# Kernel optimization log

Hardware: AMD Instinct MI355X
Metric: run time of the kernel (lower is better)

## Reference

```python
import jax, jax.numpy as jnp
import numpy as np

NUM_CLASSES = 80
NUM_PRIORS = 3
STRIDES = (8, 16, 32)
ANCHORS = (((10, 13), (16, 30), (33, 23)),
           ((30, 61), (62, 45), (59, 119)),
           ((116, 90), (156, 198), (373, 326)))
PRE_TOP_K = 1000
KEEP_TOP_K = 100
IOU_THR = 0.65
SCORE_THR = 0.25
IMG = 640
CLS_OFFSET = 4096.0  # class-offset trick for batched (class-aware) NMS


def _make_priors():
    priors, strides = [], []
    for lvl, s in enumerate(STRIDES):
        fs = IMG // s
        ys, xs = np.meshgrid(np.arange(fs), np.arange(fs), indexing='ij')
        cx = (xs * s).astype(np.float32)[..., None]
        cy = (ys * s).astype(np.float32)[..., None]
        anc = np.asarray(ANCHORS[lvl], np.float32)  # [3,2]
        cx = np.broadcast_to(cx, (fs, fs, NUM_PRIORS))
        cy = np.broadcast_to(cy, (fs, fs, NUM_PRIORS))
        w = np.broadcast_to(anc[None, None, :, 0], (fs, fs, NUM_PRIORS))
        h = np.broadcast_to(anc[None, None, :, 1], (fs, fs, NUM_PRIORS))
        box = np.stack([cx - w / 2, cy - h / 2, cx + w / 2, cy + h / 2], -1).reshape(-1, 4)
        priors.append(box)
        strides.append(np.full((box.shape[0],), s, np.float32))
    return jnp.asarray(np.concatenate(priors)), jnp.asarray(np.concatenate(strides))


def setup_inputs() -> dict:
    key = jax.random.key(0)
    ks = jax.random.split(key, 9)
    shapes = {
        'cls0': (32, 240, 80, 80), 'cls1': (32, 240, 40, 40), 'cls2': (32, 240, 20, 20),
        'bbox0': (32, 12, 80, 80), 'bbox1': (32, 12, 40, 40), 'bbox2': (32, 12, 20, 20),
        'obj0': (32, 3, 80, 80), 'obj1': (32, 3, 40, 40), 'obj2': (32, 3, 20, 20),
    }
    inp = {n: jax.random.normal(k, s, dtype=jnp.float32) for (n, s), k in zip(shapes.items(), ks)}
    priors, strides = _make_priors()
    inp['priors'] = priors
    inp['strides'] = strides
    return inp


def _flatten(x, last):  # [B,C,H,W] -> [B, H*W*priors, last]
    B = x.shape[0]
    return jnp.transpose(x, (0, 2, 3, 1)).reshape(B, -1, last)


def _decode_yolov5(priors, preds, strides):
    # priors [N,4] (x1,y1,x2,y2), preds [B,N,4], strides [N]
    p = jax.nn.sigmoid(preds)
    cx = (priors[:, 0] + priors[:, 2]) * 0.5
    cy = (priors[:, 1] + priors[:, 3]) * 0.5
    w = priors[:, 2] - priors[:, 0]
    h = priors[:, 3] - priors[:, 1]
    xc = (p[..., 0] - 0.5) * 2.0 * strides + cx
    yc = (p[..., 1] - 0.5) * 2.0 * strides + cy
    wp = (p[..., 2] * 2.0) ** 2 * w
    hp = (p[..., 3] * 2.0) ** 2 * h
    return jnp.stack([xc - wp * 0.5, yc - hp * 0.5, xc + wp * 0.5, yc + hp * 0.5], -1)


def _pairwise_iou(b):  # b [K,4]
    area = (b[:, 2] - b[:, 0]) * (b[:, 3] - b[:, 1])
    lt = jnp.maximum(b[:, None, :2], b[None, :, :2])
    rb = jnp.minimum(b[:, None, 2:], b[None, :, 2:])
    wh = jnp.clip(rb - lt, 0.0)
    inter = wh[..., 0] * wh[..., 1]
    return inter / (area[:, None] + area[None, :] - inter + 1e-7)


def _nms_single(boxes, scores):
    # boxes [N,4], scores [N,C]
    flat = scores.reshape(-1)
    top_s, top_i = jax.lax.top_k(flat, PRE_TOP_K)  # sorted desc
    anchor = top_i // NUM_CLASSES
    label = top_i % NUM_CLASSES
    b = boxes[anchor]  # [K,4]
    bo = b + label.astype(boxes.dtype)[:, None] * CLS_OFFSET
    iou = _pairwise_iou(bo)
    valid = top_s > SCORE_THR
    idxs = jnp.arange(PRE_TOP_K)

    def body(i, supp):
        keep_i = jnp.logical_not(supp[i])
        return jnp.where(keep_i & (iou[i] > IOU_THR) & (idxs > i), True, supp)

    supp = jax.lax.fori_loop(0, PRE_TOP_K, body, jnp.logical_not(valid))
    keep = jnp.logical_not(supp) & valid
    k_scores = jnp.where(keep, top_s, 0.0)
    det_s, det_i = jax.lax.top_k(k_scores, KEEP_TOP_K)
    det_b = b[det_i]
    det_l = label[det_i]
    num = jnp.minimum(jnp.sum(keep.astype(jnp.int32)), KEEP_TOP_K)
    return num, det_b, det_s, det_l


def reference(cls0, cls1, cls2, bbox0, bbox1, bbox2, obj0, obj1, obj2, priors, strides):
    cls = jnp.concatenate([_flatten(c, NUM_CLASSES) for c in (cls0, cls1, cls2)], axis=1)
    scores = jax.nn.sigmoid(cls)  # [B,N,C]
    bp = jnp.concatenate([_flatten(b, 4) for b in (bbox0, bbox1, bbox2)], axis=1)
    obj = jnp.concatenate([_flatten(o, 1)[..., 0] for o in (obj0, obj1, obj2)], axis=1)
    scores = scores * jax.nn.sigmoid(obj)[..., None]
    bboxes = _decode_yolov5(priors, bp, strides)  # [B,N,4]
    num, det_b, det_s, det_l = jax.vmap(_nms_single)(bboxes, scores)
    return num, det_b, det_s, det_l
```

## Files before the change

### kernel.cpp

```cpp
#include <hip/hip_runtime.h>
#include <stdint.h>

#define NCLS 80
#define CELLS 8400
#define PRE 1000
#define KEEP 100
#define CAP 4096
#define NBINS 16384
#define NIMG 32
#define SUBS 8
#define SUBCAP 2048
#define GBINS 4096
#define COMPCAP 2048
#define T0 0.75f
#define SCREEN 1.0886f

__device__ __forceinline__ float sigm(float x) { return 1.0f / (1.0f + __expf(-x)); }

__device__ __forceinline__ void lvlinfo(int cell, int& li, int& loc, int& HW) {
  if (cell < 6400)      { li = 0; loc = cell;        HW = 6400; }
  else if (cell < 8000) { li = 1; loc = cell - 6400; HW = 1600; }
  else                  { li = 2; loc = cell - 8000; HW = 400;  }
}

__global__ __launch_bounds__(256) void k_pass1(
    const float* __restrict__ cls0, const float* __restrict__ cls1, const float* __restrict__ cls2,
    const float* __restrict__ obj0, const float* __restrict__ obj1, const float* __restrict__ obj2,
    uint32_t* __restrict__ cnt75, uint64_t* __restrict__ cand75) {
  const int b = blockIdx.y;
  const int bx = blockIdx.x;
  const int sb = bx >> 1;
  const int h  = bx & 1;
  const int c0cell = (sb * 256 + threadIdx.x) * 4;
  if (c0cell >= CELLS) return;
  int li, loc, HW; lvlinfo(c0cell, li, loc, HW);
  const float* cls = li == 0 ? cls0 : (li == 1 ? cls1 : cls2);
  const float* obj = li == 0 ? obj0 : (li == 1 ? obj1 : obj2);

  float4 o0 = *(const float4*)(obj + ((size_t)b * 3 + 0) * HW + loc);
  float4 o1 = *(const float4*)(obj + ((size_t)b * 3 + 1) * HW + loc);
  float4 o2 = *(const float4*)(obj + ((size_t)b * 3 + 2) * HW + loc);
  float os[3][4];
  os[0][0] = sigm(o0.x); os[0][1] = sigm(o0.y); os[0][2] = sigm(o0.z); os[0][3] = sigm(o0.w);
  os[1][0] = sigm(o1.x); os[1][1] = sigm(o1.y); os[1][2] = sigm(o1.z); os[1][3] = sigm(o1.w);
  os[2][0] = sigm(o2.x); os[2][1] = sigm(o2.y); os[2][2] = sigm(o2.z); os[2][3] = sigm(o2.w);

  const int sub = bx & (SUBS - 1);
  for (int p = 0; p < 3; ++p) {
    const float* cp = cls + ((size_t)b * 240 + p * 80 + h * 40) * HW + loc;
    for (int gq = 0; gq < 5; ++gq) {
      float4 v[8];
#pragma unroll
      for (int u = 0; u < 8; ++u)
        v[u] = *(const float4*)(cp + (size_t)(gq * 8 + u) * HW);
#pragma unroll
      for (int u = 0; u < 8; ++u) {
        const int c = h * 40 + gq * 8 + u;
        float vv[4] = { v[u].x, v[u].y, v[u].z, v[u].w };
#pragma unroll
        for (int k = 0; k < 4; ++k) {
          if (vv[k] > SCREEN) {
            float s = sigm(vv[k]) * os[p][k];
            if (s > T0) {
              uint32_t slot = atomicAdd(&cnt75[b * SUBS + sub], 1u);
              if (slot < SUBCAP) {
                uint32_t flat = (uint32_t)(((c0cell + k) * 3 + p) * 80 + c);
                cand75[((size_t)(b * SUBS + sub)) * SUBCAP + slot] =
                    ((uint64_t)__float_as_uint(s) << 32) | (uint64_t)(0xFFFFFFFFu - flat);
              }
            }
          }
        }
      }
    }
  }
}

__global__ __launch_bounds__(1024) void k_gather(
    const uint64_t* __restrict__ cand75, const uint32_t* __restrict__ cnt75,
    uint32_t* __restrict__ flags,
    const float* __restrict__ bbox0, const float* __restrict__ bbox1, const float* __restrict__ bbox2,
    const float* __restrict__ priors, const float* __restrict__ strides,
    float* __restrict__ topS, int* __restrict__ topLab, float* __restrict__ topBox,
    uint32_t* __restrict__ nvArr) {
  __shared__ uint32_t hist[GBINS];
  __shared__ uint64_t comp[COMPCAP];
  __shared__ uint32_t seg[64];
  __shared__ uint32_t ncomp_s, cb_s;
  const int b = blockIdx.x;
  const int tid = threadIdx.x;
  uint32_t tot = 0; bool bad = false;
  for (int s = 0; s < SUBS; ++s) {
    uint32_t cc = cnt75[b * SUBS + s];
    tot += cc;
    if (cc > SUBCAP) bad = true;
  }
  if (tot < (uint32_t)PRE) bad = true;
  if (bad) { if (tid == 0) flags[b] = 1u; return; }

  for (int i = tid; i < GBINS; i += 1024) hist[i] = 0;
  if (tid == 0) ncomp_s = 0;
  __syncthreads();
  for (int s = 0; s < SUBS; ++s) {
    uint32_t c = cnt75[b * SUBS + s];
    const uint64_t* src = cand75 + ((size_t)(b * SUBS + s)) * SUBCAP;
    for (int i = tid; i < (int)c; i += 1024) {
      uint32_t hi = (uint32_t)(src[i] >> 32);
      uint32_t bin = (hi - 0x3F400000u) >> 10;
      if (bin > GBINS - 1) bin = GBINS - 1;
      atomicAdd(&hist[bin], 1u);
    }
  }
  __syncthreads();
  if (tid < 64) {
    uint32_t s = 0;
    for (int k = 0; k < 64; ++k) s += hist[tid * 64 + k];
    seg[tid] = s;
  }
  __syncthreads();
  if (tid == 0) {
    uint32_t acc = 0; int segi = 0;
    for (int i = 63; i >= 0; --i) {
      if (acc + seg[i] >= (uint32_t)PRE) { segi = i; break; }
      acc += seg[i];
    }
    uint32_t cb = 0;
    for (int k = 63; k >= 0; --k) {
      acc += hist[segi * 64 + k];
      if (acc >= (uint32_t)PRE) { cb = (uint32_t)(segi * 64 + k); break; }
    }
    cb_s = cb;
  }
  __syncthreads();
  const uint32_t cb = cb_s;
  for (int s = 0; s < SUBS; ++s) {
    uint32_t c = cnt75[b * SUBS + s];
    const uint64_t* src = cand75 + ((size_t)(b * SUBS + s)) * SUBCAP;
    for (int i = tid; i < (int)c; i += 1024) {
      uint64_t key = src[i];
      uint32_t hi = (uint32_t)(key >> 32);
      uint32_t bin = (hi - 0x3F400000u) >> 10;
      if (bin > GBINS - 1) bin = GBINS - 1;
      if (bin >= cb) {
        uint32_t pos = atomicAdd(&ncomp_s, 1u);
        if (pos < COMPCAP) comp[pos] = key;
      }
    }
  }
  __syncthreads();
  const uint32_t ncomp = ncomp_s;
  if (ncomp > COMPCAP) { if (tid == 0) flags[b] = 1u; return; }
  for (int i = tid; i < COMPCAP; i += 1024) if (i >= (int)ncomp) comp[i] = 0ull;
  __syncthreads();
  for (int k = 2; k <= COMPCAP; k <<= 1) {
    for (int j = k >> 1; j > 0; j >>= 1) {
      for (int i = tid; i < COMPCAP; i += 1024) {
        int p = i ^ j;
        if (p > i) {
          uint64_t a = comp[i], c = comp[p];
          bool asc = (i & k) != 0;
          if (asc ? (a > c) : (a < c)) { comp[i] = c; comp[p] = a; }
        }
      }
      __syncthreads();
    }
  }
  if (tid == 0) nvArr[b] = (uint32_t)PRE;
  for (int t = tid; t < PRE; t += 1024) {
    uint64_t key = comp[t];
    float sc = __uint_as_float((uint32_t)(key >> 32));
    uint32_t flat = 0xFFFFFFFFu - (uint32_t)(key & 0xFFFFFFFFull);
    uint32_t n = flat / 80u; int lab = (int)(flat - n * 80u);
    uint32_t g = n / 3u; uint32_t p = n - g * 3u;
    int li, loc, HW; lvlinfo((int)g, li, loc, HW);
    const float* bb = li == 0 ? bbox0 : (li == 1 ? bbox1 : bbox2);
    size_t o = ((size_t)b * 12 + p * 4) * HW + loc;
    float p0 = sigm(bb[o]);
    float p1 = sigm(bb[o + (size_t)HW]);
    float p2 = sigm(bb[o + 2 * (size_t)HW]);
    float p3 = sigm(bb[o + 3 * (size_t)HW]);
    float4 pr = *(const float4*)(priors + (size_t)n * 4);
    float st = strides[n];
    float cx = (pr.x + pr.z) * 0.5f, cy = (pr.y + pr.w) * 0.5f;
    float w = pr.z - pr.x, hh = pr.w - pr.y;
    float xc = (p0 - 0.5f) * 2.0f * st + cx;
    float yc = (p1 - 0.5f) * 2.0f * st + cy;
    float wp = p2 * 2.0f; wp = wp * wp * w;
    float hp = p3 * 2.0f; hp = hp * hp * hh;
    topS[(size_t)b * PRE + t] = sc;
    topLab[(size_t)b * PRE + t] = lab;
    *(float4*)(topBox + ((size_t)b * PRE + t) * 4) =
        make_float4(xc - wp * 0.5f, yc - hp * 0.5f, xc + wp * 0.5f, yc + hp * 0.5f);
  }
}

__global__ __launch_bounds__(256) void k_hist_fb(
    const float* __restrict__ cls0, const float* __restrict__ cls1, const float* __restrict__ cls2,
    const float* __restrict__ obj0, const float* __restrict__ obj1, const float* __restrict__ obj2,
    uint32_t* __restrict__ hist, const uint32_t* __restrict__ flags) {
  const int b = blockIdx.y;
  if (flags[b] == 0u) return;
  __shared__ uint32_t h[NBINS];
  for (int i = threadIdx.x; i < NBINS; i += 256) h[i] = 0;
  __syncthreads();
  const int c0 = (blockIdx.x * 256 + threadIdx.x) * 4;
  if (c0 < CELLS) {
    int li, loc, HW; lvlinfo(c0, li, loc, HW);
    const float* cls = li == 0 ? cls0 : (li == 1 ? cls1 : cls2);
    const float* obj = li == 0 ? obj0 : (li == 1 ? obj1 : obj2);
    float os[3][4];
#pragma unroll
    for (int p = 0; p < 3; ++p) {
      float4 o = *(const float4*)(obj + ((size_t)b * 3 + p) * HW + loc);
      os[p][0] = sigm(o.x); os[p][1] = sigm(o.y); os[p][2] = sigm(o.z); os[p][3] = sigm(o.w);
    }
    for (int p = 0; p < 3; ++p) {
      const float* cp = cls + ((size_t)b * 240 + p * 80) * HW + loc;
      for (int c = 0; c < 80; ++c) {
        float4 v = *(const float4*)(cp + (size_t)c * HW);
        float sv[4] = { sigm(v.x) * os[p][0], sigm(v.y) * os[p][1],
                        sigm(v.z) * os[p][2], sigm(v.w) * os[p][3] };
#pragma unroll
        for (int k = 0; k < 4; ++k) {
          if (sv[k] > 0.25f) {
            uint32_t key = (__float_as_uint(sv[k]) - 0x3E800000u) >> 10;
            if (key > NBINS - 1) key = NBINS - 1;
            atomicAdd(&h[key], 1u);
          }
        }
      }
    }
  }
  __syncthreads();
  for (int i = threadIdx.x; i < NBINS; i += 256) {
    uint32_t v = h[i];
    if (v) atomicAdd(&hist[(size_t)b * NBINS + i], v);
  }
}

__global__ __launch_bounds__(256) void k_cutoff_fb(const uint32_t* __restrict__ hist,
                                                   uint32_t* __restrict__ cutoff,
                                                   const uint32_t* __restrict__ flags) {
  const int b = blockIdx.x;
  if (flags[b] == 0u) return;
  __shared__ uint32_t seg[256];
  const uint32_t* hb = hist + (size_t)b * NBINS;
  uint32_t s = 0;
  for (int k = 0; k < 64; ++k) s += hb[threadIdx.x * 64 + k];
  seg[threadIdx.x] = s;
  __syncthreads();
  if (threadIdx.x == 0) {
    uint32_t acc = 0; int segi = -1;
    for (int i = 255; i >= 0; --i) {
      if (acc + seg[i] >= (uint32_t)PRE) { segi = i; break; }
      acc += seg[i];
    }
    uint32_t cut = 0;
    if (segi >= 0) {
      for (int k = 63; k >= 0; --k) {
        acc += hb[segi * 64 + k];
        if (acc >= (uint32_t)PRE) { cut = (uint32_t)(segi * 64 + k); break; }
      }
    }
    cutoff[b] = cut;
  }
}

__global__ __launch_bounds__(256) void k_collect_fb(
    const float* __restrict__ cls0, const float* __restrict__ cls1, const float* __restrict__ cls2,
    const float* __restrict__ obj0, const float* __restrict__ obj1, const float* __restrict__ obj2,
    const uint32_t* __restrict__ cutoff, uint32_t* __restrict__ candCount,
    uint64_t* __restrict__ cand, const uint32_t* __restrict__ flags) {
  const int b = blockIdx.y;
  if (flags[b] == 0u) return;
  const int c0 = (blockIdx.x * 256 + threadIdx.x) * 4;
  if (c0 >= CELLS) return;
  const uint32_t cut = cutoff[b];
  int li, loc, HW; lvlinfo(c0, li, loc, HW);
  const float* cls = li == 0 ? cls0 : (li == 1 ? cls1 : cls2);
  const float* obj = li == 0 ? obj0 : (li == 1 ? obj1 : obj2);
  float os[3][4];
#pragma unroll
  for (int p = 0; p < 3; ++p) {
    float4 o = *(const float4*)(obj + ((size_t)b * 3 + p) * HW + loc);
    os[p][0] = sigm(o.x); os[p][1] = sigm(o.y); os[p][2] = sigm(o.z); os[p][3] = sigm(o.w);
  }
  for (int p = 0; p < 3; ++p) {
    const float* cp = cls + ((size_t)b * 240 + p * 80) * HW + loc;
    for (int c = 0; c < 80; ++c) {
      float4 v = *(const float4*)(cp + (size_t)c * HW);
      float sv[4] = { sigm(v.x) * os[p][0], sigm(v.y) * os[p][1],
                      sigm(v.z) * os[p][2], sigm(v.w) * os[p][3] };
#pragma unroll
      for (int k = 0; k < 4; ++k) {
        float sk = sv[k];
        if (sk > 0.25f) {
          uint32_t key = (__float_as_uint(sk) - 0x3E800000u) >> 10;
          if (key >= cut) {
            uint32_t pos = atomicAdd(&candCount[b], 1u);
            if (pos < CAP) {
              uint32_t flat = (uint32_t)((((c0 + k) * 3 + p) * 80) + c);
              cand[(size_t)b * CAP + pos] =
                  ((uint64_t)__float_as_uint(sk) << 32) | (uint64_t)(0xFFFFFFFFu - flat);
            }
          }
        }
      }
    }
  }
}

__global__ __launch_bounds__(1024) void k_sort_decode_fb(
    const uint64_t* __restrict__ cand, const uint32_t* __restrict__ candCount,
    const float* __restrict__ bbox0, const float* __restrict__ bbox1, const float* __restrict__ bbox2,
    const float* __restrict__ priors, const float* __restrict__ strides,
    float* __restrict__ topS, int* __restrict__ topLab, float* __restrict__ topBox,
    uint32_t* __restrict__ nvArr, const uint32_t* __restrict__ flags) {
  const int b = blockIdx.x;
  if (flags[b] == 0u) return;
  __shared__ uint64_t s[CAP];
  uint32_t cnt = candCount[b]; if (cnt > (uint32_t)CAP) cnt = CAP;
  for (int i = threadIdx.x; i < CAP; i += 1024)
    s[i] = (i < (int)cnt) ? cand[(size_t)b * CAP + i] : 0ull;
  __syncthreads();
  for (int k = 2; k <= CAP; k <<= 1) {
    for (int j = k >> 1; j > 0; j >>= 1) {
      for (int i = threadIdx.x; i < CAP; i += 1024) {
        int p = i ^ j;
        if (p > i) {
          uint64_t a = s[i], c = s[p];
          bool asc = (i & k) != 0;
          if (asc ? (a > c) : (a < c)) { s[i] = c; s[p] = a; }
        }
      }
      __syncthreads();
    }
  }
  const int NV = (int)(cnt < (uint32_t)PRE ? cnt : (uint32_t)PRE);
  if (threadIdx.x == 0) nvArr[b] = (uint32_t)NV;
  for (int t = threadIdx.x; t < PRE; t += 1024) {
    float sc = 0.0f; int lab = 0; float b0 = 0, b1 = 0, b2v = 0, b3 = 0;
    if (t < NV) {
      uint64_t key = s[t];
      sc = __uint_as_float((uint32_t)(key >> 32));
      uint32_t flat = 0xFFFFFFFFu - (uint32_t)(key & 0xFFFFFFFFull);
      uint32_t n = flat / 80u; lab = (int)(flat - n * 80u);
      uint32_t g = n / 3u; uint32_t p = n - g * 3u;
      int li, loc, HW; lvlinfo((int)g, li, loc, HW);
      const float* bb = li == 0 ? bbox0 : (li == 1 ? bbox1 : bbox2);
      size_t o = ((size_t)b * 12 + p * 4) * HW + loc;
      float p0 = sigm(bb[o]);
      float p1 = sigm(bb[o + (size_t)HW]);
      float p2 = sigm(bb[o + 2 * (size_t)HW]);
      float p3 = sigm(bb[o + 3 * (size_t)HW]);
      float4 pr = *(const float4*)(priors + (size_t)n * 4);
      float st = strides[n];
      float cx = (pr.x + pr.z) * 0.5f, cy = (pr.y + pr.w) * 0.5f;
      float w = pr.z - pr.x, hh = pr.w - pr.y;
      float xc = (p0 - 0.5f) * 2.0f * st + cx;
      float yc = (p1 - 0.5f) * 2.0f * st + cy;
      float wp = p2 * 2.0f; wp = wp * wp * w;
      float hp = p3 * 2.0f; hp = hp * hp * hh;
      b0 = xc - wp * 0.5f; b1 = yc - hp * 0.5f; b2v = xc + wp * 0.5f; b3 = yc + hp * 0.5f;
    }
    topS[(size_t)b * PRE + t] = sc;
    topLab[(size_t)b * PRE + t] = lab;
    *(float4*)(topBox + ((size_t)b * PRE + t) * 4) = make_float4(b0, b1, b2v, b3);
  }
}

__global__ __launch_bounds__(256) void k_iou(
    const float* __restrict__ topBox, const int* __restrict__ topLab,
    const uint32_t* __restrict__ nvArr, uint64_t* __restrict__ mask) {
  __shared__ float4 bx[PRE];
  __shared__ int lb[PRE];
  const int b = blockIdx.y;
  const int NV = (int)nvArr[b];
  for (int i = threadIdx.x; i < PRE; i += 256) {
    bx[i] = *(const float4*)(topBox + ((size_t)b * PRE + i) * 4);
    lb[i] = topLab[(size_t)b * PRE + i];
  }
  __syncthreads();
  for (int task = blockIdx.x * 256 + threadIdx.x; task < PRE * 16; task += gridDim.x * 256) {
    const int i = task >> 4, w = task & 15;
    uint64_t m = 0;
    if (i < NV) {
      const float4 a = bx[i]; const int la = lb[i];
      const float areaA = (a.z - a.x) * (a.w - a.y);
      const int j0 = w << 6;
      const int jend = (j0 + 64 < NV) ? j0 + 64 : NV;
      for (int j = (j0 > i + 1 ? j0 : i + 1); j < jend; ++j) {
        if (lb[j] != la) continue;
        const float4 c = bx[j];
        float xx1 = fmaxf(a.x, c.x), yy1 = fmaxf(a.y, c.y);
        float xx2 = fminf(a.z, c.z), yy2 = fminf(a.w, c.w);
        float iw = fmaxf(xx2 - xx1, 0.0f), ih = fmaxf(yy2 - yy1, 0.0f);
        float inter = iw * ih;
        float areaB = (c.z - c.x) * (c.w - c.y);
        float iou = inter / (areaA + areaB - inter + 1e-7f);
        if (iou > 0.65f) m |= (1ull << (j - j0));
      }
    }
    mask[((size_t)b * PRE + i) * 16 + w] = m;
  }
}

__global__ __launch_bounds__(256) void k_scan_out(
    const uint64_t* __restrict__ mask, const float* __restrict__ topS,
    const int* __restrict__ topLab, const float* __restrict__ topBox,
    const uint32_t* __restrict__ nvArr, float* __restrict__ out) {
  __shared__ uint64_t rows[PRE * 16];
  __shared__ uint64_t keepw[16];
  __shared__ uint32_t pref[17];
  const int b = blockIdx.x;
  const int NV = (int)nvArr[b];
  for (int i = threadIdx.x; i < NV * 16; i += 256) rows[i] = mask[(size_t)b * PRE * 16 + i];
  __syncthreads();
  if (threadIdx.x < 64) {
    const int lane = threadIdx.x;
    uint64_t remv = 0, kw = 0;
    for (int w0 = 0; w0 * 64 < NV; ++w0) {
      uint64_t cur = (uint64_t)__shfl((unsigned long long)remv, w0);
      const int ie = (w0 * 64 + 64 < NV) ? w0 * 64 + 64 : NV;
      for (int i = w0 * 64; i < ie; ++i) {
        const int bi = i & 63;
        if (!((cur >> bi) & 1ull)) {
          uint64_t rl = rows[i * 16 + (lane & 15)];
          cur |= rows[i * 16 + w0];
          if (lane < 16) remv |= rl;
          if (lane == w0) kw |= (1ull << bi);
        }
      }
    }
    if (lane < 16) keepw[lane] = kw;
  }
  __syncthreads();
  if (threadIdx.x == 0) {
    uint32_t a = 0;
    for (int w = 0; w < 16; ++w) { pref[w] = a; a += (uint32_t)__popcll((unsigned long long)keepw[w]); }
    pref[16] = a;
  }
  __syncthreads();
  const uint32_t total = pref[16];
  const uint32_t num = total < (uint32_t)KEEP ? total : (uint32_t)KEEP;
  float* o_num = out;
  float* o_box = out + NIMG;
  float* o_s   = out + NIMG + NIMG * KEEP * 4;
  float* o_l   = o_s + NIMG * KEEP;
  if (threadIdx.x == 0) o_num[b] = (float)num;
  const int zstart = NV < KEEP ? NV : KEEP;
  for (int sidx = zstart + threadIdx.x; sidx < KEEP; sidx += 256) {
    ((float4*)o_box)[b * KEEP + sidx] = make_float4(0, 0, 0, 0);
    o_s[b * KEEP + sidx] = 0.0f;
    o_l[b * KEEP + sidx] = 0.0f;
  }
  for (int j = threadIdx.x; j < NV; j += 256) {
    const int wi = j >> 6, bi = j & 63;
    const uint64_t kword = keepw[wi];
    const int isk = (int)((kword >> bi) & 1ull);
    const uint32_t below = pref[wi] + (uint32_t)__popcll((unsigned long long)(kword & ((1ull << bi) - 1ull)));
    const uint32_t slot = isk ? below : (total + (uint32_t)j - below);
    if (slot < (uint32_t)KEEP) {
      ((float4*)o_box)[b * KEEP + slot] = *(const float4*)(topBox + ((size_t)b * PRE + j) * 4);
      o_s[b * KEEP + slot] = isk ? topS[(size_t)b * PRE + j] : 0.0f;
      o_l[b * KEEP + slot] = (float)topLab[(size_t)b * PRE + j];
    }
  }
}

extern "C" void kernel_launch(void* const* d_in, const int* in_sizes, int n_in,
                              void* d_out, int out_size, void* d_ws, size_t ws_size,
                              hipStream_t stream) {
  (void)in_sizes; (void)n_in; (void)out_size; (void)ws_size;
  const float* cls0 = (const float*)d_in[0];
  const float* cls1 = (const float*)d_in[1];
  const float* cls2 = (const float*)d_in[2];
  const float* bbox0 = (const float*)d_in[3];
  const float* bbox1 = (const float*)d_in[4];
  const float* bbox2 = (const float*)d_in[5];
  const float* obj0 = (const float*)d_in[6];
  const float* obj1 = (const float*)d_in[7];
  const float* obj2 = (const float*)d_in[8];
  const float* priors = (const float*)d_in[9];
  const float* strides = (const float*)d_in[10];
  float* out = (float*)d_out;

  char* ws = (char*)d_ws;
  size_t off = 0;
  auto alloc = [&](size_t bytes) -> void* {
    void* p = ws + off;
    off = (off + bytes + 255) & ~(size_t)255;
    return p;
  };
  uint32_t* small     = (uint32_t*)alloc(4096);
  uint32_t* flags     = small;
  uint32_t* cnt75     = small + 32;
  uint32_t* candCount = small + 288;
  uint32_t* cutoff    = small + 320;
  uint32_t* nvArr     = small + 352;
  uint64_t* cand75    = (uint64_t*)alloc((size_t)NIMG * SUBS * SUBCAP * 8);
  uint32_t* hist      = (uint32_t*)alloc((size_t)NIMG * NBINS * 4);
  uint64_t* cand      = (uint64_t*)alloc((size_t)NIMG * CAP * 8);
  float*    topS      = (float*)alloc((size_t)NIMG * PRE * 4);
  int*      topLab    = (int*)alloc((size_t)NIMG * PRE * 4);
  float*    topBox    = (float*)alloc((size_t)NIMG * PRE * 16);
  uint64_t* maskbuf   = (uint64_t*)alloc((size_t)NIMG * PRE * 16 * 8);

  hipMemsetAsync(small, 0, 4096, stream);
  hipMemsetAsync(hist, 0, (size_t)NIMG * NBINS * 4, stream);

  k_pass1<<<dim3(18, NIMG), 256, 0, stream>>>(cls0, cls1, cls2, obj0, obj1, obj2,
                                              cnt75, cand75);
  k_gather<<<NIMG, 1024, 0, stream>>>(cand75, cnt75, flags, bbox0, bbox1, bbox2,
                                      priors, strides, topS, topLab, topBox, nvArr);
  dim3 gScan(9, NIMG);
  k_hist_fb<<<gScan, 256, 0, stream>>>(cls0, cls1, cls2, obj0, obj1, obj2, hist, flags);
  k_cutoff_fb<<<NIMG, 256, 0, stream>>>(hist, cutoff, flags);
  k_collect_fb<<<gScan, 256, 0, stream>>>(cls0, cls1, cls2, obj0, obj1, obj2,
                                          cutoff, candCount, cand, flags);
  k_sort_decode_fb<<<NIMG, 1024, 0, stream>>>(cand, candCount, bbox0, bbox1, bbox2,
                                              priors, strides, topS, topLab, topBox, nvArr, flags);
  k_iou<<<dim3(63, NIMG), 256, 0, stream>>>(topBox, topLab, nvArr, maskbuf);
  k_scan_out<<<NIMG, 256, 0, stream>>>(maskbuf, topS, topLab, topBox, nvArr, out);
}
```

Baseline: 421.6 us.

## Double-buffer pass1 loads, shrink gather sort, fuse IoU with scan, gate hist zeroing

Pass1 now software-pipelines class-channel loads across two register buffers and skips a group early when its max is below the screen threshold. The gather bitonic sort uses 1024 elements when the candidate count fits. The 2MB histogram memset becomes a kernel that zeroes only when some image needs the fallback path. The IoU-mask and scan kernels are fused into one block per image that keeps the mask in shared memory, which removes a global round-trip but drops from 63x32 blocks to 32 blocks for the IoU work.

```diff
diff --git a/kernel.cpp b/kernel.cpp
--- a/kernel.cpp
+++ b/kernel.cpp
@@ -46,34 +46,41 @@
   os[2][0] = sigm(o2.x); os[2][1] = sigm(o2.y); os[2][2] = sigm(o2.z); os[2][3] = sigm(o2.w);
 
   const int sub = bx & (SUBS - 1);
+
+#define LD(dst, GQ) { _Pragma("unroll") for (int u = 0; u < 8; ++u) \
+    dst[u] = *(const float4*)(cp + (size_t)((GQ) * 8 + u) * HW); }
+#define PR(src, GQ) { \
+    float mx = fmaxf(fmaxf(src[0].x, src[0].y), fmaxf(src[0].z, src[0].w)); \
+    _Pragma("unroll") for (int u = 1; u < 8; ++u) \
+      mx = fmaxf(mx, fmaxf(fmaxf(src[u].x, src[u].y), fmaxf(src[u].z, src[u].w))); \
+    if (mx > SCREEN) { \
+      _Pragma("unroll") for (int u = 0; u < 8; ++u) { \
+        const int c = h * 40 + (GQ) * 8 + u; \
+        float vv[4] = { src[u].x, src[u].y, src[u].z, src[u].w }; \
+        _Pragma("unroll") for (int k = 0; k < 4; ++k) { \
+          if (vv[k] > SCREEN) { \
+            float s = sigm(vv[k]) * os[p][k]; \
+            if (s > T0) { \
+              uint32_t slot = atomicAdd(&cnt75[b * SUBS + sub], 1u); \
+              if (slot < SUBCAP) { \
+                uint32_t flat = (uint32_t)(((c0cell + k) * 3 + p) * 80 + c); \
+                cand75[((size_t)(b * SUBS + sub)) * SUBCAP + slot] = \
+                    ((uint64_t)__float_as_uint(s) << 32) | (uint64_t)(0xFFFFFFFFu - flat); \
+              } } } } } } }
+
+#pragma unroll
   for (int p = 0; p < 3; ++p) {
     const float* cp = cls + ((size_t)b * 240 + p * 80 + h * 40) * HW + loc;
-    for (int gq = 0; gq < 5; ++gq) {
-      float4 v[8];
-#pragma unroll
-      for (int u = 0; u < 8; ++u)
-        v[u] = *(const float4*)(cp + (size_t)(gq * 8 + u) * HW);
-#pragma unroll
-      for (int u = 0; u < 8; ++u) {
-        const int c = h * 40 + gq * 8 + u;
-        float vv[4] = { v[u].x, v[u].y, v[u].z, v[u].w };
-#pragma unroll
-        for (int k = 0; k < 4; ++k) {
-          if (vv[k] > SCREEN) {
-            float s = sigm(vv[k]) * os[p][k];
-            if (s > T0) {
-              uint32_t slot = atomicAdd(&cnt75[b * SUBS + sub], 1u);
-              if (slot < SUBCAP) {
-                uint32_t flat = (uint32_t)(((c0cell + k) * 3 + p) * 80 + c);
-                cand75[((size_t)(b * SUBS + sub)) * SUBCAP + slot] =
-                    ((uint64_t)__float_as_uint(s) << 32) | (uint64_t)(0xFFFFFFFFu - flat);
-              }
-            }
-          }
-        }
-      }
-    }
-  }
+    float4 va[8], vb[8];
+    LD(va, 0)
+    LD(vb, 1) PR(va, 0)
+    LD(va, 2) PR(vb, 1)
+    LD(vb, 3) PR(va, 2)
+    LD(va, 4) PR(vb, 3)
+    PR(va, 4)
+  }
+#undef LD
+#undef PR
 }
 
 __global__ __launch_bounds__(1024) void k_gather(
@@ -150,11 +157,12 @@
   __syncthreads();
   const uint32_t ncomp = ncomp_s;
   if (ncomp > COMPCAP) { if (tid == 0) flags[b] = 1u; return; }
-  for (int i = tid; i < COMPCAP; i += 1024) if (i >= (int)ncomp) comp[i] = 0ull;
-  __syncthreads();
-  for (int k = 2; k <= COMPCAP; k <<= 1) {
+  const int N = (ncomp <= 1024u) ? 1024 : COMPCAP;
+  for (int i = tid; i < N; i += 1024) if (i >= (int)ncomp) comp[i] = 0ull;
+  __syncthreads();
+  for (int k = 2; k <= N; k <<= 1) {
     for (int j = k >> 1; j > 0; j >>= 1) {
-      for (int i = tid; i < COMPCAP; i += 1024) {
+      for (int i = tid; i < N; i += 1024) {
         int p = i ^ j;
         if (p > i) {
           uint64_t a = comp[i], c = comp[p];
@@ -194,6 +202,21 @@
   }
 }
 
+__global__ __launch_bounds__(256) void k_zero_hist(uint32_t* __restrict__ hist,
+                                                   const uint32_t* __restrict__ flags) {
+  __shared__ uint32_t any;
+  if (threadIdx.x == 0) {
+    uint32_t a = 0;
+    for (int i = 0; i < NIMG; ++i) a |= flags[i];
+    any = a;
+  }
+  __syncthreads();
+  if (!any) return;
+  const int total = NIMG * NBINS;
+  for (int i = blockIdx.x * 256 + threadIdx.x; i < total; i += gridDim.x * 256)
+    hist[i] = 0;
+}
+
 __global__ __launch_bounds__(256) void k_hist_fb(
     const float* __restrict__ cls0, const float* __restrict__ cls1, const float* __restrict__ cls2,
     const float* __restrict__ obj0, const float* __restrict__ obj1, const float* __restrict__ obj2,
@@ -369,19 +392,23 @@
   }
 }
 
-__global__ __launch_bounds__(256) void k_iou(
+__global__ __launch_bounds__(256) void k_iou_scan(
     const float* __restrict__ topBox, const int* __restrict__ topLab,
-    const uint32_t* __restrict__ nvArr, uint64_t* __restrict__ mask) {
+    const float* __restrict__ topS, const uint32_t* __restrict__ nvArr,
+    float* __restrict__ out) {
   __shared__ float4 bx[PRE];
   __shared__ int lb[PRE];
-  const int b = blockIdx.y;
+  __shared__ uint64_t rows[PRE * 16];
+  __shared__ uint64_t keepw[16];
+  __shared__ uint32_t pref[17];
+  const int b = blockIdx.x;
   const int NV = (int)nvArr[b];
   for (int i = threadIdx.x; i < PRE; i += 256) {
     bx[i] = *(const float4*)(topBox + ((size_t)b * PRE + i) * 4);
     lb[i] = topLab[(size_t)b * PRE + i];
   }
   __syncthreads();
-  for (int task = blockIdx.x * 256 + threadIdx.x; task < PRE * 16; task += gridDim.x * 256) {
+  for (int task = threadIdx.x; task < PRE * 16; task += 256) {
     const int i = task >> 4, w = task & 15;
     uint64_t m = 0;
     if (i < NV) {
@@ -401,20 +428,8 @@
         if (iou > 0.65f) m |= (1ull << (j - j0));
       }
     }
-    mask[((size_t)b * PRE + i) * 16 + w] = m;
-  }
-}
-
-__global__ __launch_bounds__(256) void k_scan_out(
-    const uint64_t* __restrict__ mask, const float* __restrict__ topS,
-    const int* __restrict__ topLab, const float* __restrict__ topBox,
-    const uint32_t* __restrict__ nvArr, float* __restrict__ out) {
-  __shared__ uint64_t rows[PRE * 16];
-  __shared__ uint64_t keepw[16];
-  __shared__ uint32_t pref[17];
-  const int b = blockIdx.x;
-  const int NV = (int)nvArr[b];
-  for (int i = threadIdx.x; i < NV * 16; i += 256) rows[i] = mask[(size_t)b * PRE * 16 + i];
+    rows[i * 16 + w] = m;
+  }
   __syncthreads();
   if (threadIdx.x < 64) {
     const int lane = threadIdx.x;
@@ -461,9 +476,9 @@
     const uint32_t below = pref[wi] + (uint32_t)__popcll((unsigned long long)(kword & ((1ull << bi) - 1ull)));
     const uint32_t slot = isk ? below : (total + (uint32_t)j - below);
     if (slot < (uint32_t)KEEP) {
-      ((float4*)o_box)[b * KEEP + slot] = *(const float4*)(topBox + ((size_t)b * PRE + j) * 4);
+      ((float4*)o_box)[b * KEEP + slot] = bx[j];
       o_s[b * KEEP + slot] = isk ? topS[(size_t)b * PRE + j] : 0.0f;
-      o_l[b * KEEP + slot] = (float)topLab[(size_t)b * PRE + j];
+      o_l[b * KEEP + slot] = (float)lb[j];
     }
   }
 }
@@ -504,15 +519,14 @@
   float*    topS      = (float*)alloc((size_t)NIMG * PRE * 4);
   int*      topLab    = (int*)alloc((size_t)NIMG * PRE * 4);
   float*    topBox    = (float*)alloc((size_t)NIMG * PRE * 16);
-  uint64_t* maskbuf   = (uint64_t*)alloc((size_t)NIMG * PRE * 16 * 8);
 
   hipMemsetAsync(small, 0, 4096, stream);
-  hipMemsetAsync(hist, 0, (size_t)NIMG * NBINS * 4, stream);
 
   k_pass1<<<dim3(18, NIMG), 256, 0, stream>>>(cls0, cls1, cls2, obj0, obj1, obj2,
                                               cnt75, cand75);
   k_gather<<<NIMG, 1024, 0, stream>>>(cand75, cnt75, flags, bbox0, bbox1, bbox2,
                                       priors, strides, topS, topLab, topBox, nvArr);
+  k_zero_hist<<<256, 256, 0, stream>>>(hist, flags);
   dim3 gScan(9, NIMG);
   k_hist_fb<<<gScan, 256, 0, stream>>>(cls0, cls1, cls2, obj0, obj1, obj2, hist, flags);
   k_cutoff_fb<<<NIMG, 256, 0, stream>>>(hist, cutoff, flags);
@@ -520,6 +534,5 @@
                                           cutoff, candCount, cand, flags);
   k_sort_decode_fb<<<NIMG, 1024, 0, stream>>>(cand, candCount, bbox0, bbox1, bbox2,
                                               priors, strides, topS, topLab, topBox, nvArr, flags);
-  k_iou<<<dim3(63, NIMG), 256, 0, stream>>>(topBox, topLab, nvArr, maskbuf);
-  k_scan_out<<<NIMG, 256, 0, stream>>>(maskbuf, topS, topLab, topBox, nvArr, out);
-}
+  k_iou_scan<<<NIMG, 256, 0, stream>>>(topBox, topLab, topS, nvArr, out);
+}
```

After: 830.1 us. 96.9% more time.

## Split pass1 per prior, shrink bitonic sort, lazy hist zeroing, branchless NMS scan

Applied to the files above, without the earlier changes.

The first pass grid now launches one block per (cell tile, prior, class half), tripling the block count for more parallelism on the bandwidth-bound class scan. The gather bitonic sort runs on 1024 entries when the candidate count fits, halving the sort work. The histogram memset is replaced by a kernel that clears it only when some image took the fallback path. The NMS scan loop becomes branchless with masks. The risks are an extra launch and more obj reloads, and the sub-bucket index now comes from a different block mapping, which could change atomic contention.

```diff
diff --git a/kernel.cpp b/kernel.cpp
--- a/kernel.cpp
+++ b/kernel.cpp
@@ -29,45 +29,40 @@
     uint32_t* __restrict__ cnt75, uint64_t* __restrict__ cand75) {
   const int b = blockIdx.y;
   const int bx = blockIdx.x;
-  const int sb = bx >> 1;
-  const int h  = bx & 1;
+  const int sb = bx / 6;
+  const int r  = bx - sb * 6;
+  const int h  = r & 1;
+  const int p  = r >> 1;
   const int c0cell = (sb * 256 + threadIdx.x) * 4;
   if (c0cell >= CELLS) return;
   int li, loc, HW; lvlinfo(c0cell, li, loc, HW);
   const float* cls = li == 0 ? cls0 : (li == 1 ? cls1 : cls2);
   const float* obj = li == 0 ? obj0 : (li == 1 ? obj1 : obj2);
 
-  float4 o0 = *(const float4*)(obj + ((size_t)b * 3 + 0) * HW + loc);
-  float4 o1 = *(const float4*)(obj + ((size_t)b * 3 + 1) * HW + loc);
-  float4 o2 = *(const float4*)(obj + ((size_t)b * 3 + 2) * HW + loc);
-  float os[3][4];
-  os[0][0] = sigm(o0.x); os[0][1] = sigm(o0.y); os[0][2] = sigm(o0.z); os[0][3] = sigm(o0.w);
-  os[1][0] = sigm(o1.x); os[1][1] = sigm(o1.y); os[1][2] = sigm(o1.z); os[1][3] = sigm(o1.w);
-  os[2][0] = sigm(o2.x); os[2][1] = sigm(o2.y); os[2][2] = sigm(o2.z); os[2][3] = sigm(o2.w);
+  float4 ov = *(const float4*)(obj + ((size_t)b * 3 + p) * HW + loc);
+  float os[4] = { sigm(ov.x), sigm(ov.y), sigm(ov.z), sigm(ov.w) };
 
   const int sub = bx & (SUBS - 1);
-  for (int p = 0; p < 3; ++p) {
-    const float* cp = cls + ((size_t)b * 240 + p * 80 + h * 40) * HW + loc;
-    for (int gq = 0; gq < 5; ++gq) {
-      float4 v[8];
-#pragma unroll
-      for (int u = 0; u < 8; ++u)
-        v[u] = *(const float4*)(cp + (size_t)(gq * 8 + u) * HW);
-#pragma unroll
-      for (int u = 0; u < 8; ++u) {
-        const int c = h * 40 + gq * 8 + u;
-        float vv[4] = { v[u].x, v[u].y, v[u].z, v[u].w };
-#pragma unroll
-        for (int k = 0; k < 4; ++k) {
-          if (vv[k] > SCREEN) {
-            float s = sigm(vv[k]) * os[p][k];
-            if (s > T0) {
-              uint32_t slot = atomicAdd(&cnt75[b * SUBS + sub], 1u);
-              if (slot < SUBCAP) {
-                uint32_t flat = (uint32_t)(((c0cell + k) * 3 + p) * 80 + c);
-                cand75[((size_t)(b * SUBS + sub)) * SUBCAP + slot] =
-                    ((uint64_t)__float_as_uint(s) << 32) | (uint64_t)(0xFFFFFFFFu - flat);
-              }
+  const float* cp = cls + ((size_t)b * 240 + p * 80 + h * 40) * HW + loc;
+  for (int gq = 0; gq < 5; ++gq) {
+    float4 v[8];
+#pragma unroll
+    for (int u = 0; u < 8; ++u)
+      v[u] = *(const float4*)(cp + (size_t)(gq * 8 + u) * HW);
+#pragma unroll
+    for (int u = 0; u < 8; ++u) {
+      const int c = h * 40 + gq * 8 + u;
+      float vv[4] = { v[u].x, v[u].y, v[u].z, v[u].w };
+#pragma unroll
+      for (int k = 0; k < 4; ++k) {
+        if (vv[k] > SCREEN) {
+          float s = sigm(vv[k]) * os[k];
+          if (s > T0) {
+            uint32_t slot = atomicAdd(&cnt75[b * SUBS + sub], 1u);
+            if (slot < SUBCAP) {
+              uint32_t flat = (uint32_t)(((c0cell + k) * 3 + p) * 80 + c);
+              cand75[((size_t)(b * SUBS + sub)) * SUBCAP + slot] =
+                  ((uint64_t)__float_as_uint(s) << 32) | (uint64_t)(0xFFFFFFFFu - flat);
             }
           }
         }
@@ -150,11 +145,12 @@
   __syncthreads();
   const uint32_t ncomp = ncomp_s;
   if (ncomp > COMPCAP) { if (tid == 0) flags[b] = 1u; return; }
-  for (int i = tid; i < COMPCAP; i += 1024) if (i >= (int)ncomp) comp[i] = 0ull;
-  __syncthreads();
-  for (int k = 2; k <= COMPCAP; k <<= 1) {
+  const int N = (ncomp <= 1024u) ? 1024 : COMPCAP;
+  for (int i = tid; i < N; i += 1024) if (i >= (int)ncomp) comp[i] = 0ull;
+  __syncthreads();
+  for (int k = 2; k <= N; k <<= 1) {
     for (int j = k >> 1; j > 0; j >>= 1) {
-      for (int i = tid; i < COMPCAP; i += 1024) {
+      for (int i = tid; i < N; i += 1024) {
         int p = i ^ j;
         if (p > i) {
           uint64_t a = comp[i], c = comp[p];
@@ -194,6 +190,21 @@
   }
 }
 
+__global__ __launch_bounds__(256) void k_zero_hist(uint32_t* __restrict__ hist,
+                                                   const uint32_t* __restrict__ flags) {
+  __shared__ uint32_t any;
+  if (threadIdx.x == 0) {
+    uint32_t a = 0;
+    for (int i = 0; i < NIMG; ++i) a |= flags[i];
+    any = a;
+  }
+  __syncthreads();
+  if (!any) return;
+  const int total = NIMG * NBINS;
+  for (int i = blockIdx.x * 256 + threadIdx.x; i < total; i += gridDim.x * 256)
+    hist[i] = 0;
+}
+
 __global__ __launch_bounds__(256) void k_hist_fb(
     const float* __restrict__ cls0, const float* __restrict__ cls1, const float* __restrict__ cls2,
     const float* __restrict__ obj0, const float* __restrict__ obj1, const float* __restrict__ obj2,
@@ -424,12 +435,12 @@
       const int ie = (w0 * 64 + 64 < NV) ? w0 * 64 + 64 : NV;
       for (int i = w0 * 64; i < ie; ++i) {
         const int bi = i & 63;
-        if (!((cur >> bi) & 1ull)) {
-          uint64_t rl = rows[i * 16 + (lane & 15)];
-          cur |= rows[i * 16 + w0];
-          if (lane < 16) remv |= rl;
-          if (lane == w0) kw |= (1ull << bi);
-        }
+        uint64_t rl = rows[i * 16 + (lane & 15)];
+        uint64_t cw = rows[i * 16 + w0];
+        const uint64_t keepm = ((cur >> bi) & 1ull) ? 0ull : ~0ull;
+        cur |= cw & keepm;
+        remv |= rl & keepm;
+        kw |= (lane == w0) ? ((1ull << bi) & keepm) : 0ull;
       }
     }
     if (lane < 16) keepw[lane] = kw;
@@ -507,12 +518,12 @@
   uint64_t* maskbuf   = (uint64_t*)alloc((size_t)NIMG * PRE * 16 * 8);
 
   hipMemsetAsync(small, 0, 4096, stream);
-  hipMemsetAsync(hist, 0, (size_t)NIMG * NBINS * 4, stream);
-
-  k_pass1<<<dim3(18, NIMG), 256, 0, stream>>>(cls0, cls1, cls2, obj0, obj1, obj2,
+
+  k_pass1<<<dim3(54, NIMG), 256, 0, stream>>>(cls0, cls1, cls2, obj0, obj1, obj2,
                                               cnt75, cand75);
   k_gather<<<NIMG, 1024, 0, stream>>>(cand75, cnt75, flags, bbox0, bbox1, bbox2,
                                       priors, strides, topS, topLab, topBox, nvArr);
+  k_zero_hist<<<256, 256, 0, stream>>>(hist, flags);
   dim3 gScan(9, NIMG);
   k_hist_fb<<<gScan, 256, 0, stream>>>(cls0, cls1, cls2, obj0, obj1, obj2, hist, flags);
   k_cutoff_fb<<<NIMG, 256, 0, stream>>>(hist, cutoff, flags);
```

New measurement: 372.4 us. 11.7% less time.
